# Kernel tuning notes

Hardware: AMD Instinct MI355X
Metric: run time of the kernel (lower is better)

Reference implementation:

```python
import jax, jax.numpy as jnp
import numpy as np

DIM = 1024
HEADS = 16
DIM_HEAD = 64
INNER = HEADS * DIM_HEAD  # 1024
SCALE = 1.0 / DIM_HEAD ** 0.5


def setup_inputs() -> dict:
    key = jax.random.key(0)
    ks = jax.random.split(key, 5)
    x = jax.random.normal(ks[0], (4, 2048, DIM), dtype=jnp.float32)
    # nn.Linear weights stored as [out, in]; we keep [in, out] for x @ W
    Wq = jax.random.normal(ks[1], (DIM, INNER), dtype=jnp.float32) * (1.0 / np.sqrt(DIM))
    Wkv = jax.random.normal(ks[2], (DIM, 2 * INNER), dtype=jnp.float32) * (1.0 / np.sqrt(DIM))
    Wo = jax.random.normal(ks[3], (INNER, DIM), dtype=jnp.float32) * (1.0 / np.sqrt(INNER))
    bo = jax.random.normal(ks[4], (DIM,), dtype=jnp.float32) * 0.01
    return {"x": x, "Wq": Wq, "Wkv": Wkv, "Wo": Wo, "bo": bo}


def reference(x, Wq, Wkv, Wo, bo):
    b, n, _ = x.shape
    q = x @ Wq                      # [b, n, inner]
    kv = x @ Wkv                    # [b, n, 2*inner]
    k, v = jnp.split(kv, 2, axis=2)
    # 'b n (h d) -> b h n d'
    q = q.reshape(b, n, HEADS, DIM_HEAD).transpose(0, 2, 1, 3)
    k = k.reshape(b, n, HEADS, DIM_HEAD).transpose(0, 2, 1, 3)
    v = v.reshape(b, n, HEADS, DIM_HEAD).transpose(0, 2, 1, 3)
    scores = jnp.einsum('bhid,bhjd->bhij', q, k) * SCALE  # [b,h,n,n]
    attn = jax.nn.softmax(scores, axis=-1)
    out = jnp.einsum('bhij,bhjd->bhid', attn, v)          # [b,h,n,d]
    out = out.transpose(0, 2, 1, 3).reshape(b, n, INNER)  # 'b h n d -> b n (h d)'
    return out @ Wo + bo
```

## Files before the change

### kernel.cpp

```cpp
#include <hip/hip_runtime.h>
#include <hip/hip_bf16.h>

typedef unsigned short u16;
typedef unsigned int u32;
typedef __attribute__((ext_vector_type(8))) short s8v;
typedef __attribute__((ext_vector_type(4))) float f4v;
typedef __attribute__((ext_vector_type(4))) unsigned short u16x4;

#define MFMA16(a,b,c) __builtin_amdgcn_mfma_f32_16x16x32_bf16((a),(b),(c),0,0,0)

#define TOKENS 8192
#define SEQ    2048
#define NH     16
#define DH     64
#define DIMK   1024
#define QPRE   0.18033688f

#if defined(__has_builtin)
#if __has_builtin(__builtin_amdgcn_exp2f)
#define EXP2(x) __builtin_amdgcn_exp2f(x)
#else
#define EXP2(x) __expf((x) * 0.69314718f)
#endif
#else
#define EXP2(x) __expf((x) * 0.69314718f)
#endif

__device__ __forceinline__ u16 f2bf(float x){
  union { float f; u32 u; } v; v.f = x;
  u32 r = v.u + 0x7FFFu + ((v.u >> 16) & 1u);
  return (u16)(r >> 16);
}

__device__ __forceinline__ void gld16(const u16* g, u16* s){
  __builtin_amdgcn_global_load_lds(
      (const __attribute__((address_space(1))) unsigned int*)(const void*)g,
      (__attribute__((address_space(3))) unsigned int*)(void*)s,
      16, 0, 0);
}

__global__ __launch_bounds__(256) void k_cast(const float* __restrict__ src,
                                              u16* __restrict__ dst){
  int i = (blockIdx.x * 256 + threadIdx.x) * 4;
  float4 v = *(const float4*)(src + i);
  u16x4 vh;
  float a[4] = {v.x, v.y, v.z, v.w};
#pragma unroll
  for (int j = 0; j < 4; j++) vh[j] = f2bf(a[j]);
  *(u16x4*)(dst + i) = vh;
}

__global__ __launch_bounds__(256) void k_transpose(const float* __restrict__ s0, int c0,
                                                   const float* __restrict__ s1, int c1,
                                                   int K, u16* __restrict__ dh){
  __shared__ float tile[64][65];
  int nb = blockIdx.x * 64, kb = blockIdx.y * 64;
  int tr = threadIdx.x >> 6, tc = threadIdx.x & 63;
#pragma unroll
  for (int i = 0; i < 16; i++){
    int k = kb + tr + i * 4, n = nb + tc;
    float v = (n < c0) ? s0[(size_t)k * c0 + n] : s1[(size_t)k * c1 + (n - c0)];
    tile[tr + i * 4][tc] = v;
  }
  __syncthreads();
#pragma unroll
  for (int i = 0; i < 16; i++){
    int nl = tr + i * 4, kl = tc;
    dh[(size_t)(nb + nl) * K + (kb + kl)] = f2bf(tile[kl][nl]);
  }
}

__global__ __launch_bounds__(256, 3) void k_gemm_qkv(
    const u16* __restrict__ A, const u16* __restrict__ B,
    u16* __restrict__ Qh, u16* __restrict__ Kh, u16* __restrict__ Vth)
{
  __shared__ u16 sA[2][256*32];
  __shared__ u16 sB[2][128*32];
  const int tid = threadIdx.x, wave = tid >> 6, lane = tid & 63;
  const int lm = lane & 15, quad = lane >> 4;

  const int bid = blockIdx.x;
  const int xcd = bid & 7, slot = bid >> 3;
  const int nt = slot >> 2;
  const int mloc = slot & 3;
  const int m0 = (xcd * 4 + mloc) * 256, n0 = nt * 128;

  const int cof = (lane & 3) * 8;
  const int rsub = lane >> 2;

  f4v acc[4][8];
#pragma unroll
  for (int i = 0; i < 4; i++)
#pragma unroll
    for (int j = 0; j < 8; j++) acc[i][j] = (f4v){0.f, 0.f, 0.f, 0.f};

  for (int kc = 0; kc < 16; kc++){
    int k = kc * 64;
#pragma unroll
    for (int cc = 0; cc < 2; cc++){
#pragma unroll
      for (int half = 0; half < 4; half++){
        int rb = wave * 64 + half * 16;
        gld16(A + (size_t)(m0 + rb + rsub) * DIMK + k + cc * 32 + cof, &sA[cc][rb * 32]);
      }
#pragma unroll
      for (int half = 0; half < 2; half++){
        int rb = wave * 32 + half * 16;
        gld16(B + (size_t)(n0 + rb + rsub) * DIMK + k + cc * 32 + cof, &sB[cc][rb * 32]);
      }
    }
    __syncthreads();

#pragma unroll
    for (int cc = 0; cc < 2; cc++){
      s8v ah[4], bh[8];
#pragma unroll
      for (int i = 0; i < 4; i++)
        ah[i] = *(const s8v*)&sA[cc][(wave * 64 + i * 16 + lm) * 32 + quad * 8];
#pragma unroll
      for (int j = 0; j < 8; j++)
        bh[j] = *(const s8v*)&sB[cc][(j * 16 + lm) * 32 + quad * 8];
#pragma unroll
      for (int i = 0; i < 4; i++)
#pragma unroll
        for (int j = 0; j < 8; j++)
          acc[i][j] = MFMA16(ah[i], bh[j], acc[i][j]);
    }
    __syncthreads();
  }

#pragma unroll
  for (int i = 0; i < 4; i++)
#pragma unroll
    for (int j = 0; j < 8; j++){
      int gn = n0 + j * 16 + lm;
#pragma unroll
      for (int r = 0; r < 4; r++){
        int gm = m0 + wave * 64 + i * 16 + quad * 4 + r;
        float v = acc[i][j][r];
        if (gn < 1024){
          Qh[(size_t)gm * DIMK + gn] = f2bf(v * QPRE);
        } else if (gn < 2048){
          Kh[(size_t)gm * DIMK + (gn - 1024)] = f2bf(v);
        } else {
          int df = gn - 2048;
          int hh = df >> 6, dd = df & 63;
          int bb = gm >> 11, ii = gm & 2047;
          int ip = (ii & ~31) | (((ii & 15) << 1) | ((ii >> 4) & 1));
          Vth[(size_t)((bb * NH + hh) * DH + dd) * SEQ + ip] = f2bf(v);
        }
      }
    }
}

__global__ __launch_bounds__(256) void k_gemm_op(
    const u16* __restrict__ A, const u16* __restrict__ B,
    const float* __restrict__ bias, float* __restrict__ Cf)
{
  __shared__ u16 sA[2][128*32], sB[2][128*32];
  const int tid = threadIdx.x, wave = tid >> 6, lane = tid & 63;
  const int lm = lane & 15, quad = lane >> 4;

  const int bid = blockIdx.x;
  const int xcd = bid & 7, slot = bid >> 3;
  const int nt = slot >> 3, mloc = slot & 7;
  const int m0 = (xcd * 8 + mloc) * 128, n0 = nt * 128;

  const int cof = (lane & 3) * 8;
  const int rsub = lane >> 2;

  f4v acc[4][4];
#pragma unroll
  for (int i = 0; i < 4; i++)
#pragma unroll
    for (int j = 0; j < 4; j++) acc[i][j] = (f4v){0.f, 0.f, 0.f, 0.f};

  const int wm = (wave >> 1) * 64, wn = (wave & 1) * 64;

  for (int kc = 0; kc < 16; kc++){
    int k = kc * 64;
#pragma unroll
    for (int cc = 0; cc < 2; cc++)
#pragma unroll
      for (int half = 0; half < 2; half++){
        int rb = wave * 32 + half * 16;
        gld16(A + (size_t)(m0 + rb + rsub) * DIMK + k + cc * 32 + cof, &sA[cc][rb * 32]);
        gld16(B + (size_t)(n0 + rb + rsub) * DIMK + k + cc * 32 + cof, &sB[cc][rb * 32]);
      }
    __syncthreads();

#pragma unroll
    for (int cc = 0; cc < 2; cc++){
      s8v ah[4], bh[4];
#pragma unroll
      for (int i = 0; i < 4; i++){
        ah[i] = *(const s8v*)&sA[cc][(wm + i * 16 + lm) * 32 + quad * 8];
        bh[i] = *(const s8v*)&sB[cc][(wn + i * 16 + lm) * 32 + quad * 8];
      }
#pragma unroll
      for (int i = 0; i < 4; i++)
#pragma unroll
        for (int j = 0; j < 4; j++)
          acc[i][j] = MFMA16(ah[i], bh[j], acc[i][j]);
    }
    __syncthreads();
  }

#pragma unroll
  for (int i = 0; i < 4; i++)
#pragma unroll
    for (int j = 0; j < 4; j++){
      int gn = n0 + wn + j * 16 + lm;
      float bv = bias[gn];
#pragma unroll
      for (int r = 0; r < 4; r++){
        int gm = m0 + wm + i * 16 + quad * 4 + r;
        Cf[(size_t)gm * DIMK + gn] = acc[i][j][r] + bv;
      }
    }
}

__global__ __launch_bounds__(256, 4) void k_attn(
    const u16* __restrict__ Qh, const u16* __restrict__ Kh, const u16* __restrict__ Vth,
    u16* __restrict__ Oh)
{
  __shared__ u16 sK[2*64*32];
  __shared__ u16 sV[2*64*32];
  __shared__ u16 sP[2*128*32];
  u32* sPd = (u32*)sP;

  const int bid = blockIdx.x;
  const int xcd = bid & 7, slot = bid >> 3;
  const int g = xcd * 8 + (slot >> 4);
  const int qt = slot & 15;
  const int b = g >> 4, h = g & 15;

  const int tid = threadIdx.x, wave = tid >> 6, lane = tid & 63;
  const int lm = lane & 15, quad = lane >> 4;
  const int tok0 = b * SEQ + qt * 128;
  const int cof = (lane & 3) * 8;
  const int rsub = lane >> 2;

  s8v qf[2][2];
#pragma unroll
  for (int c = 0; c < 2; c++)
#pragma unroll
    for (int ifr = 0; ifr < 2; ifr++){
      size_t ga = (size_t)(tok0 + wave * 32 + ifr * 16 + lm) * DIMK + h * DH + c * 32 + quad * 8;
      qf[c][ifr] = *(const s8v*)(Qh + ga);
    }

  const f4v fz = (f4v){0.f, 0.f, 0.f, 0.f};

  float lpart[2][4];
  f4v oacc[2][4];
#pragma unroll
  for (int ifr = 0; ifr < 2; ifr++){
#pragma unroll
    for (int r = 0; r < 4; r++) lpart[ifr][r] = 0.f;
#pragma unroll
    for (int fd = 0; fd < 4; fd++) oacc[ifr][fd] = (f4v){0.f, 0.f, 0.f, 0.f};
  }

  for (int kt = 0; kt < 32; kt++){
    int j0 = kt * 64;
#pragma unroll
    for (int c = 0; c < 2; c++){
      size_t gk = (size_t)(b * SEQ + j0 + wave * 16 + rsub) * DIMK + h * DH + c * 32 + cof;
      gld16(Kh + gk, &sK[c * 2048 + wave * 512]);
      size_t gv = (size_t)((b * NH + h) * DH + wave * 16 + rsub) * SEQ + j0 + c * 32 + cof;
      gld16(Vth + gv, &sV[c * 2048 + wave * 512]);
    }
    __syncthreads();

    f4v s[2][4];
#pragma unroll
    for (int fn = 0; fn < 4; fn++){
      s8v kh0 = *(const s8v*)&sK[0 * 2048 + (fn * 16 + lm) * 32 + quad * 8];
      s8v kh1 = *(const s8v*)&sK[1 * 2048 + (fn * 16 + lm) * 32 + quad * 8];
#pragma unroll
      for (int ifr = 0; ifr < 2; ifr++){
        s[ifr][fn] = MFMA16(qf[0][ifr], kh0, fz);
        s[ifr][fn] = MFMA16(qf[1][ifr], kh1, s[ifr][fn]);
      }
    }

#pragma unroll
    for (int ifr = 0; ifr < 2; ifr++){
#pragma unroll
      for (int fn = 0; fn < 4; fn++)
#pragma unroll
        for (int r = 0; r < 4; r++)
          s[ifr][fn][r] = EXP2(s[ifr][fn][r]);
      int rowb = wave * 32 + ifr * 16 + quad * 4;
#pragma unroll
      for (int r = 0; r < 4; r++)
#pragma unroll
        for (int jc = 0; jc < 2; jc++){
          union { float f; u32 u; } a0, a1;
          a0.f = s[ifr][jc * 2 + 0][r];
          a1.f = s[ifr][jc * 2 + 1][r];
          lpart[ifr][r] += a0.f + a1.f;
          sPd[jc * 2048 + (rowb + r) * 16 + lm] = __builtin_amdgcn_perm(a1.u, a0.u, 0x07060302);
        }
    }

#pragma unroll
    for (int c = 0; c < 2; c++)
#pragma unroll
      for (int ifr = 0; ifr < 2; ifr++){
        s8v ph = *(const s8v*)&sP[c * 4096 + (wave * 32 + ifr * 16 + lm) * 32 + quad * 8];
#pragma unroll
        for (int fd = 0; fd < 4; fd++){
          s8v vh = *(const s8v*)&sV[c * 2048 + (fd * 16 + lm) * 32 + quad * 8];
          oacc[ifr][fd] = MFMA16(ph, vh, oacc[ifr][fd]);
        }
      }
    __syncthreads();
  }

#pragma unroll
  for (int ifr = 0; ifr < 2; ifr++){
#pragma unroll
    for (int off = 1; off < 16; off <<= 1)
#pragma unroll
      for (int r = 0; r < 4; r++)
        lpart[ifr][r] += __shfl_xor(lpart[ifr][r], off, 64);
    float inv[4];
#pragma unroll
    for (int r = 0; r < 4; r++) inv[r] = 1.f / lpart[ifr][r];
#pragma unroll
    for (int fd = 0; fd < 4; fd++){
      int dcol = h * DH + fd * 16 + lm;
#pragma unroll
      for (int r = 0; r < 4; r++){
        int tok = tok0 + wave * 32 + ifr * 16 + quad * 4 + r;
        Oh[(size_t)tok * DIMK + dcol] = f2bf(oacc[ifr][fd][r] * inv[r]);
      }
    }
  }
}

extern "C" void kernel_launch(void* const* d_in, const int* in_sizes, int n_in,
                              void* d_out, int out_size, void* d_ws, size_t ws_size,
                              hipStream_t stream) {
  const float* x   = (const float*)d_in[0];
  const float* Wq  = (const float*)d_in[1];
  const float* Wkv = (const float*)d_in[2];
  const float* Wo  = (const float*)d_in[3];
  const float* bo  = (const float*)d_in[4];
  float* out = (float*)d_out;

  char* ws = (char*)d_ws;
  size_t off = 0;
  auto alloc = [&](size_t bytes) -> u16* {
    u16* p = (u16*)(ws + off);
    off += (bytes + 255) & ~(size_t)255;
    return p;
  };
  const size_t TK2 = (size_t)TOKENS * DIMK * 2;
  u16* xh  = alloc(TK2);
  u16* Wh  = alloc((size_t)3072 * DIMK * 2);
  u16* WOh = alloc((size_t)1024 * DIMK * 2);
  u16* Qh  = alloc(TK2);
  u16* Kh  = alloc(TK2);
  u16* Vth = alloc(TK2);
  u16* Oh  = alloc(TK2);

  k_cast<<<dim3((TOKENS * DIMK) / 1024), 256, 0, stream>>>(x, xh);
  k_transpose<<<dim3(48, 16), 256, 0, stream>>>(Wq, 1024, Wkv, 2048, DIMK, Wh);
  k_transpose<<<dim3(16, 16), 256, 0, stream>>>(Wo, 1024, Wo, 1024, DIMK, WOh);
  k_gemm_qkv<<<dim3(24 * 32), 256, 0, stream>>>(xh, Wh, Qh, Kh, Vth);
  k_attn<<<dim3(16 * NH * 4), 256, 0, stream>>>(Qh, Kh, Vth, Oh);
  k_gemm_op<<<dim3(8 * 64), 256, 0, stream>>>(Oh, WOh, bo, out);
}
```

Measured before the change: 313.9 us.

## Rewrite QKV GEMM as 256x256 tile, 8-wave ping-pong pipelined kernel

Restructures the QKV projection GEMM from 256x128 tiles with 4 waves into 256x256 tiles with 8 waves (2x4 wave grid), halving the block count. Global-to-LDS staging is split into half-tiles that are interleaved with MFMA phases, using double-buffered register fragments, explicit vmcnt waits, fine-grained barriers, s_setprio around the MFMAs, and an XOR swizzle on the LDS layout to avoid bank conflicts. The aim is to overlap loads with compute and raise data reuse per loaded byte. The cost is heavier register and LDS pressure (128 KB LDS per block) and fragile hand-written synchronisation.

```diff
diff --git a/kernel.cpp b/kernel.cpp
--- a/kernel.cpp
+++ b/kernel.cpp
@@ -70,74 +70,90 @@
   }
 }
 
-__global__ __launch_bounds__(256, 3) void k_gemm_qkv(
+#define GQ_STAGE_A(buf,h,t) do{ \
+  gld16(As + (size_t)(h)*131072 + (size_t)(t)*64,      &lds[(buf)*32768 + (h)*8192 + w*512]); \
+  gld16(As + (size_t)(h)*131072 + (size_t)(t)*64 + 32, &lds[(buf)*32768 + (h)*8192 + 4096 + w*512]); }while(0)
+#define GQ_STAGE_B(buf,h,t) do{ \
+  gld16(Bs + (size_t)(h)*131072 + (size_t)(t)*64,      &lds[(buf)*32768 + 16384 + (h)*8192 + w*512]); \
+  gld16(Bs + (size_t)(h)*131072 + (size_t)(t)*64 + 32, &lds[(buf)*32768 + 16384 + (h)*8192 + 4096 + w*512]); }while(0)
+#define GQ_RDA(dst,buf,mh) do{ _Pragma("unroll") for (int i_ = 0; i_ < 4; i_++){ \
+  dst[i_][0] = *(const s8v*)&lds[(buf)*32768 + aRB + ((mh)*4+i_)*512]; \
+  dst[i_][1] = *(const s8v*)&lds[(buf)*32768 + aRB + 4096 + ((mh)*4+i_)*512]; } }while(0)
+#define GQ_RDB(dst,buf,nh) do{ _Pragma("unroll") for (int j_ = 0; j_ < 2; j_++){ \
+  dst[j_][0] = *(const s8v*)&lds[(buf)*32768 + bRB + ((nh)*2+j_)*512]; \
+  dst[j_][1] = *(const s8v*)&lds[(buf)*32768 + bRB + 4096 + ((nh)*2+j_)*512]; } }while(0)
+#define GQ_MMA(aS,bS,mh,nh) do{ __builtin_amdgcn_s_setprio(1); \
+  _Pragma("unroll") for (int i_ = 0; i_ < 4; i_++) \
+  _Pragma("unroll") for (int j_ = 0; j_ < 2; j_++){ \
+    acc[(mh)*4+i_][(nh)*2+j_] = MFMA16(aS[i_][0], bS[j_][0], acc[(mh)*4+i_][(nh)*2+j_]); \
+    acc[(mh)*4+i_][(nh)*2+j_] = MFMA16(aS[i_][1], bS[j_][1], acc[(mh)*4+i_][(nh)*2+j_]); } \
+  __builtin_amdgcn_s_setprio(0); }while(0)
+#define GQ_BAR() do{ asm volatile("" ::: "memory"); __builtin_amdgcn_s_barrier(); asm volatile("" ::: "memory"); }while(0)
+#define GQ_VMW2() asm volatile("s_waitcnt vmcnt(2)" ::: "memory")
+
+__global__ __launch_bounds__(512, 2) void k_gemm_qkv(
     const u16* __restrict__ A, const u16* __restrict__ B,
     u16* __restrict__ Qh, u16* __restrict__ Kh, u16* __restrict__ Vth)
 {
-  __shared__ u16 sA[2][256*32];
-  __shared__ u16 sB[2][128*32];
-  const int tid = threadIdx.x, wave = tid >> 6, lane = tid & 63;
+  __shared__ u16 lds[65536];
+  const int tid = threadIdx.x;
+  const int w = tid >> 6, lane = tid & 63;
   const int lm = lane & 15, quad = lane >> 4;
+  const int wm = w >> 2, wn = w & 3;
 
   const int bid = blockIdx.x;
   const int xcd = bid & 7, slot = bid >> 3;
   const int nt = slot >> 2;
   const int mloc = slot & 3;
-  const int m0 = (xcd * 4 + mloc) * 256, n0 = nt * 128;
-
-  const int cof = (lane & 3) * 8;
-  const int rsub = lane >> 2;
-
-  f4v acc[4][8];
-#pragma unroll
-  for (int i = 0; i < 4; i++)
-#pragma unroll
-    for (int j = 0; j < 8; j++) acc[i][j] = (f4v){0.f, 0.f, 0.f, 0.f};
-
-  for (int kc = 0; kc < 16; kc++){
-    int k = kc * 64;
-#pragma unroll
-    for (int cc = 0; cc < 2; cc++){
-#pragma unroll
-      for (int half = 0; half < 4; half++){
-        int rb = wave * 64 + half * 16;
-        gld16(A + (size_t)(m0 + rb + rsub) * DIMK + k + cc * 32 + cof, &sA[cc][rb * 32]);
-      }
-#pragma unroll
-      for (int half = 0; half < 2; half++){
-        int rb = wave * 32 + half * 16;
-        gld16(B + (size_t)(n0 + rb + rsub) * DIMK + k + cc * 32 + cof, &sB[cc][rb * 32]);
-      }
-    }
-    __syncthreads();
-
-#pragma unroll
-    for (int cc = 0; cc < 2; cc++){
-      s8v ah[4], bh[8];
-#pragma unroll
-      for (int i = 0; i < 4; i++)
-        ah[i] = *(const s8v*)&sA[cc][(wave * 64 + i * 16 + lm) * 32 + quad * 8];
-#pragma unroll
-      for (int j = 0; j < 8; j++)
-        bh[j] = *(const s8v*)&sB[cc][(j * 16 + lm) * 32 + quad * 8];
-#pragma unroll
-      for (int i = 0; i < 4; i++)
-#pragma unroll
-        for (int j = 0; j < 8; j++)
-          acc[i][j] = MFMA16(ah[i], bh[j], acc[i][j]);
-    }
-    __syncthreads();
-  }
-
-#pragma unroll
-  for (int i = 0; i < 4; i++)
-#pragma unroll
-    for (int j = 0; j < 8; j++){
-      int gn = n0 + j * 16 + lm;
+  const int m0 = (xcd * 4 + mloc) * 256, n0 = nt * 256;
+
+  const int srow = lane >> 2;
+  const int scol = ((lane & 3) ^ (((lane >> 5) & 1) << 1)) * 8;
+  const u16* As = A + (size_t)(m0 + w * 16 + srow) * DIMK + scol;
+  const u16* Bs = B + (size_t)(n0 + w * 16 + srow) * DIMK + scol;
+
+  const int swz = (lm & 8) << 1;
+  const int aRB = wm * 8192 + lm * 32 + ((quad * 8) ^ swz);
+  const int bRB = 16384 + (wn >> 1) * 8192 + (wn & 1) * 2048 + lm * 32 + ((quad * 8) ^ swz);
+
+  f4v acc[8][4];
+#pragma unroll
+  for (int i = 0; i < 8; i++)
+#pragma unroll
+    for (int j = 0; j < 4; j++) acc[i][j] = (f4v){0.f, 0.f, 0.f, 0.f};
+
+  s8v aA[4][2], aB[4][2], bA[2][2], bB[2][2];
+
+  GQ_STAGE_A(0,0,0); GQ_STAGE_A(0,1,0); GQ_STAGE_B(0,0,0); GQ_STAGE_B(0,1,0);
+  GQ_STAGE_A(1,0,1);
+  GQ_VMW2(); GQ_BAR();
+  GQ_RDA(aA,0,0); GQ_RDB(bA,0,0);
+
+  for (int it = 0; it < 8; it++){
+    const int t1 = 2 * it + 1;
+    const int t2 = (it < 7) ? 2 * it + 2 : 15;
+    const int t3 = (it < 7) ? 2 * it + 3 : 15;
+    GQ_STAGE_A(1,1,t1); GQ_BAR(); GQ_RDA(aB,0,1);                 GQ_MMA(aA,bA,0,0);
+    GQ_STAGE_B(1,0,t1); GQ_BAR(); GQ_RDB(bB,0,1);                 GQ_MMA(aB,bA,1,0);
+    GQ_STAGE_B(1,1,t1); GQ_BAR();                                 GQ_MMA(aB,bB,1,1);
+    GQ_STAGE_A(0,0,t2); GQ_VMW2(); GQ_BAR();
+                                  GQ_RDA(aB,1,0); GQ_RDB(bA,1,0); GQ_MMA(aA,bB,0,1);
+    GQ_STAGE_A(0,1,t2); GQ_BAR(); GQ_RDA(aA,1,1);                 GQ_MMA(aB,bA,0,0);
+    GQ_STAGE_B(0,0,t2); GQ_BAR(); GQ_RDB(bB,1,1);                 GQ_MMA(aA,bA,1,0);
+    GQ_STAGE_B(0,1,t2); GQ_BAR();                                 GQ_MMA(aA,bB,1,1);
+    GQ_STAGE_A(1,0,t3); GQ_VMW2(); GQ_BAR();
+                                  GQ_RDA(aA,0,0); GQ_RDB(bA,0,0); GQ_MMA(aB,bB,0,1);
+  }
+
+#pragma unroll
+  for (int ig = 0; ig < 8; ig++)
+#pragma unroll
+    for (int jg = 0; jg < 4; jg++){
+      const int gn = n0 + wn * 64 + jg * 16 + lm;
 #pragma unroll
       for (int r = 0; r < 4; r++){
-        int gm = m0 + wave * 64 + i * 16 + quad * 4 + r;
-        float v = acc[i][j][r];
+        const int gm = m0 + wm * 128 + ig * 16 + quad * 4 + r;
+        float v = acc[ig][jg][r];
         if (gn < 1024){
           Qh[(size_t)gm * DIMK + gn] = f2bf(v * QPRE);
         } else if (gn < 2048){
@@ -370,7 +386,7 @@
   k_cast<<<dim3((TOKENS * DIMK) / 1024), 256, 0, stream>>>(x, xh);
   k_transpose<<<dim3(48, 16), 256, 0, stream>>>(Wq, 1024, Wkv, 2048, DIMK, Wh);
   k_transpose<<<dim3(16, 16), 256, 0, stream>>>(Wo, 1024, Wo, 1024, DIMK, WOh);
-  k_gemm_qkv<<<dim3(24 * 32), 256, 0, stream>>>(xh, Wh, Qh, Kh, Vth);
+  k_gemm_qkv<<<dim3(384), 512, 0, stream>>>(xh, Wh, Qh, Kh, Vth);
   k_attn<<<dim3(16 * NH * 4), 256, 0, stream>>>(Qh, Kh, Vth, Oh);
   k_gemm_op<<<dim3(8 * 64), 256, 0, stream>>>(Oh, WOh, bo, out);
 }
```

After: 302.3 us. -3.7%, faster.
